# Kernel optimization log

Measured on AMD Instinct MI355X. Metric: run time of the kernel, lower is better.

Reference implementation:

```python
import jax, jax.numpy as jnp
import numpy as np

N = 50000          # nodes per node type
F = 256            # input feature dim
C = 256            # hidden_channels
H, D = 8, 32       # heads, head_dim (C = H*D)
E = 200000         # edges per edge type
OUT = 16           # out_channels
SRC = (0, 1, 0)    # edge type -> source node-type index (user,item)
DST = (1, 0, 0)    # edge type -> destination node-type index
LABELED = 1        # labeled_class = 'item'


def setup_inputs() -> dict:
    key = jax.random.key(0)
    ks = jax.random.split(key, 24)
    s = 0.06  # ~1/sqrt(256) init scale
    inp = {
        'x': jax.random.normal(ks[0], (2, N, F), jnp.float32),
        'edge_index': jax.random.randint(ks[1], (3, 2, E), 0, N, jnp.int64),
        'lin_w': jax.random.normal(ks[2], (2, F, C), jnp.float32) * s,
        'lin_b': jnp.zeros((2, C), jnp.float32),
        'k_w': jax.random.normal(ks[3], (2, C, C), jnp.float32) * s,
        'k_b': jnp.zeros((2, C), jnp.float32),
        'q_w': jax.random.normal(ks[4], (2, C, C), jnp.float32) * s,
        'q_b': jnp.zeros((2, C), jnp.float32),
        'v_w': jax.random.normal(ks[5], (2, C, C), jnp.float32) * s,
        'v_b': jnp.zeros((2, C), jnp.float32),
        'a_w': jax.random.normal(ks[6], (2, C, C), jnp.float32) * s,
        'a_b': jnp.zeros((2, C), jnp.float32),
        'skip': jnp.ones((2,), jnp.float32),
        'a_rel': jax.random.normal(ks[7], (3, H, D, D), jnp.float32) * (1.0 / np.sqrt(D)),
        'm_rel': jax.random.normal(ks[8], (3, H, D, D), jnp.float32) * (1.0 / np.sqrt(D)),
        'p_rel': jnp.ones((3, H), jnp.float32),
        'out_w': jax.random.normal(ks[9], (C, OUT), jnp.float32) * s,
        'out_b': jnp.zeros((OUT,), jnp.float32),
    }
    return inp


def _segment_softmax(alpha, idx, n):
    # alpha: [E, H], idx: [E] destination node ids
    amax = jax.ops.segment_max(alpha, idx, num_segments=n)
    amax = jnp.where(jnp.isfinite(amax), amax, 0.0)
    ex = jnp.exp(alpha - amax[idx])
    den = jax.ops.segment_sum(ex, idx, num_segments=n)
    return ex / (den[idx] + 1e-16)


def reference(x, edge_index, lin_w, lin_b, k_w, k_b, q_w, q_b, v_w, v_b,
              a_w, a_b, skip, a_rel, m_rel, p_rel, out_w, out_b):
    # per-node-type input Linear + ReLU
    h = jax.nn.relu(jnp.einsum('tnf,tfc->tnc', x, lin_w) + lin_b[:, None, :])

    def proj(w, b):
        return (jnp.einsum('tnc,tce->tne', h, w) + b[:, None, :]).reshape(2, N, H, D)

    k = proj(k_w, k_b)
    q = proj(q_w, q_b)
    v = proj(v_w, v_b)

    agg = jnp.zeros((2, N, H, D), h.dtype)
    for t in range(3):  # fixed small loop over edge types
        s, d = SRC[t], DST[t]
        src_idx, dst_idx = edge_index[t, 0], edge_index[t, 1]
        # relation-specific transforms of source keys / values
        k_rel = jnp.einsum('nhd,hde->nhe', k[s], a_rel[t])
        v_rel = jnp.einsum('nhd,hde->nhe', v[s], m_rel[t])
        # per-edge attention logits [E, H]
        alpha = (q[d][dst_idx] * k_rel[src_idx]).sum(-1) * p_rel[t] / (D ** 0.5)
        alpha = _segment_softmax(alpha, dst_idx, N)
        msg = v_rel[src_idx] * alpha[..., None]          # [E, H, D]
        agg = agg.at[d].add(jax.ops.segment_sum(msg, dst_idx, num_segments=N))

    o = agg.reshape(2, N, C)
    o = jnp.einsum('tnc,tce->tne', jax.nn.gelu(o, approximate=False), a_w) + a_b[:, None, :]
    beta = jax.nn.sigmoid(skip)[:, None, None]
    o = beta * o + (1.0 - beta) * h                      # skip connection (in == out dims)

    return o[LABELED] @ out_w + out_b                    # logits for labeled_class='item'
```

## Files before the change

kernel.cpp:

```cpp
#include <hip/hip_runtime.h>
#include <hip/hip_bf16.h>

using u16 = unsigned short;
using u32 = unsigned int;

#define NNODES 50000
#define NEDGE  200000
#define DEGCAP 64
#define NT     3125

__device__ __forceinline__ float blo2f(u32 u) { u32 v = u << 16; float f; __builtin_memcpy(&f, &v, 4); return f; }
__device__ __forceinline__ float bhi2f(u32 u) { u32 v = u & 0xffff0000u; float f; __builtin_memcpy(&f, &v, 4); return f; }
__device__ __forceinline__ u16 f2b(float f) {
  __hip_bfloat16 h = __float2bfloat16(f);
  u16 r; __builtin_memcpy(&r, &h, 2); return r;
}
__device__ __forceinline__ float gelu_exact(float x) {
  return 0.5f * x * (1.f + erff(x * 0.70710678118654752f));
}

__device__ __forceinline__ void gload16(const void* gp, void* lp) {
  __builtin_amdgcn_global_load_lds(
      (__attribute__((address_space(1))) u32*)(const_cast<void*>(gp)),
      (__attribute__((address_space(3))) u32*)lp, 16, 0, 0);
}

__device__ __forceinline__ void wait_vm0() { asm volatile("s_waitcnt vmcnt(0)" ::: "memory"); }
__device__ __forceinline__ void wait_vm2() { asm volatile("s_waitcnt vmcnt(2)" ::: "memory"); }
__device__ __forceinline__ void wait_vm4() { asm volatile("s_waitcnt vmcnt(4)" ::: "memory"); }

typedef __bf16 bh8 __attribute__((ext_vector_type(8)));
typedef float f32x4 __attribute__((ext_vector_type(4)));

struct GArg { const u16* A; const u16* B; const float* bias; u16* C; };

__device__ __forceinline__ void stage_tile(const u16* At, u16* buf, int lane) {
#pragma unroll
  for (int i = 0; i < 8; ++i) {
    const int row = i * 2 + (lane >> 5);
    const int c   = (lane & 31) ^ (row & 7);
    gload16(At + (size_t)row * 256 + c * 8, buf + i * 512 + lane * 8);
  }
}

__device__ __forceinline__ void stage_blk_bf16(const u16* At, u16* buf, int wave, int lane) {
#pragma unroll
  for (int i = 0; i < 2; ++i) {
    const int row = wave * 4 + i * 2 + (lane >> 5);
    const int c   = (lane & 31) ^ (row & 7);
    gload16(At + (size_t)row * 256 + c * 8, buf + wave * 1024 + i * 512 + lane * 8);
  }
}

__device__ __forceinline__ void stage_blk_f32(const float* At, float* buf, int wave, int lane) {
#pragma unroll
  for (int i = 0; i < 4; ++i) {
    const int row = wave * 4 + i;
    const int c   = lane ^ ((row & 7) << 1);
    gload16(At + (size_t)row * 256 + c * 4, buf + row * 256 + lane * 4);
  }
}

template <int MODE, bool F32A>
__launch_bounds__(256, 2)
__global__ void gemm_v9(GArg g0, GArg g1, GArg g2)
{
  GArg ga = (blockIdx.z == 0) ? g0 : ((blockIdx.z == 1) ? g1 : g2);
  const int tid  = threadIdx.x;
  const int lane = tid & 63;
  const int wave = tid >> 6;
  const int lr = lane & 15;
  const int lq = lane >> 4;
  const int colbase = wave * 64;

  constexpr int TW = F32A ? 8192 : 4096;
  __shared__ alignas(16) u16 lds[2][TW];
  __shared__ alignas(16) u16 pat[4][1152];
  u16* wl = &pat[wave][0];

  bh8 B[4][8];
#pragma unroll
  for (int s = 0; s < 4; ++s) {
    const u16* bp = ga.B + (size_t)(colbase + s * 16 + lr) * 256 + lq * 8;
#pragma unroll
    for (int ks = 0; ks < 8; ++ks) B[s][ks] = *(const bh8*)(bp + ks * 32);
  }
  float bias[4];
#pragma unroll
  for (int s = 0; s < 4; ++s) bias[s] = ga.bias[colbase + s * 16 + lr];

  int foff[8];
#pragma unroll
  for (int ks = 0; ks < 8; ++ks) {
    if (F32A)
      foff[ks] = lr * 256 + (((ks * 8 + lq * 2) ^ ((lr & 7) << 1)) * 4);
    else
      foff[ks] = lr * 256 + (((ks * 4 + lq) ^ (lr & 7)) * 8);
  }

  const int t0 = blockIdx.x;
  const int ts = gridDim.x;

  if (F32A) stage_blk_f32((const float*)ga.A + (size_t)t0 * 4096, (float*)&lds[0][0], wave, lane);
  else      stage_blk_bf16(ga.A + (size_t)t0 * 4096, &lds[0][0], wave, lane);
  int cur = 0;

  for (int t = t0; t < NT; t += ts) {
    const int tn = t + ts;
    if (tn < NT) {
      if (F32A) { stage_blk_f32((const float*)ga.A + (size_t)tn * 4096, (float*)&lds[cur ^ 1][0], wave, lane); wait_vm4(); }
      else      { stage_blk_bf16(ga.A + (size_t)tn * 4096, &lds[cur ^ 1][0], wave, lane); wait_vm2(); }
    } else {
      wait_vm0();
    }
    __builtin_amdgcn_s_barrier();

    bh8 ab[8];
    if (F32A) {
      const float* fbuf = (const float*)&lds[cur][0];
#pragma unroll
      for (int ks = 0; ks < 8; ++ks) {
        const f32x4 lo = *(const f32x4*)(fbuf + foff[ks]);
        const f32x4 hi = *(const f32x4*)(fbuf + foff[ks] + 4);
#pragma unroll
        for (int j = 0; j < 4; ++j) { ab[ks][j] = (__bf16)lo[j]; ab[ks][j + 4] = (__bf16)hi[j]; }
      }
    } else {
      const u16* buf = &lds[cur][0];
#pragma unroll
      for (int ks = 0; ks < 8; ++ks) ab[ks] = *(const bh8*)(buf + foff[ks]);
    }

    f32x4 acc[4];
#pragma unroll
    for (int s = 0; s < 4; ++s) acc[s] = (f32x4){0.f, 0.f, 0.f, 0.f};
#pragma unroll
    for (int ks = 0; ks < 8; ++ks) {
#pragma unroll
      for (int s = 0; s < 4; ++s)
        acc[s] = __builtin_amdgcn_mfma_f32_16x16x32_bf16(ab[ks], B[s][ks], acc[s], 0, 0, 0);
    }

#pragma unroll
    for (int s = 0; s < 4; ++s) {
#pragma unroll
      for (int r = 0; r < 4; ++r) {
        float v = acc[s][r] + bias[s];
        if (MODE == 0) v = fmaxf(v, 0.f);
        wl[(lq * 4 + r) * 72 + s * 16 + lr] = f2b(v);
      }
    }
#pragma unroll
    for (int j = 0; j < 2; ++j) {
      const int row = (lane >> 3) + j * 8;
      const int seg = lane & 7;
      const uint4 pv = *(const uint4*)(wl + row * 72 + seg * 8);
      *(uint4*)(ga.C + ((size_t)t * 16 + row) * 256 + colbase + seg * 8) = pv;
    }
    __builtin_amdgcn_s_barrier();
    cur ^= 1;
  }
}

__global__ void prep_w_k(const float* __restrict__ lin_w, const float* __restrict__ q_w,
                         const float* __restrict__ a_w, const float* __restrict__ k_w,
                         const float* __restrict__ v_w, const float* __restrict__ k_b,
                         const float* __restrict__ v_b, const float* __restrict__ a_rel,
                         const float* __restrict__ m_rel, const float* __restrict__ out_w,
                         const float* __restrict__ a_b, const float* __restrict__ out_b,
                         const float* __restrict__ skipv,
                         u16* __restrict__ lin0T, u16* __restrict__ lin1T,
                         u16* __restrict__ qT,
                         u16* __restrict__ kfT, u16* __restrict__ vfT,
                         u16* __restrict__ WcT, float* __restrict__ bfin,
                         float* __restrict__ bkf, float* __restrict__ bvf,
                         int* __restrict__ cnt)
{
  const int tid = blockIdx.x * 256 + threadIdx.x;
  const int nn = tid >> 8, kk = tid & 255;
  switch (blockIdx.y) {
    case 0: lin0T[tid] = f2b(lin_w[kk * 256 + nn]); break;
    case 1: lin1T[tid] = f2b(lin_w[65536 + kk * 256 + nn]); break;
    case 2: qT[tid] = f2b(q_w[65536 + kk * 256 + nn]); break;
    case 3: {
      const int h = nn >> 5, e = nn & 31;
      float s = 0.f;
      for (int d = 0; d < 32; ++d) s += k_w[kk * 256 + h * 32 + d] * a_rel[(h * 32 + d) * 32 + e];
      kfT[tid] = f2b(s);
      if (kk == 0) {
        float sb = 0.f;
        for (int d = 0; d < 32; ++d) sb += k_b[h * 32 + d] * a_rel[(h * 32 + d) * 32 + e];
        bkf[nn] = sb;
      }
      break;
    }
    case 4: {
      const int h = nn >> 5, e = nn & 31;
      float s = 0.f;
      for (int d = 0; d < 32; ++d) s += v_w[kk * 256 + h * 32 + d] * m_rel[(h * 32 + d) * 32 + e];
      vfT[tid] = f2b(s);
      if (kk == 0) {
        float sb = 0.f;
        for (int d = 0; d < 32; ++d) sb += v_b[h * 32 + d] * m_rel[(h * 32 + d) * 32 + e];
        bvf[nn] = sb;
      }
      break;
    }
    case 5: {
      const float beta = 1.f / (1.f + __expf(-skipv[1]));
      if (tid < 8192) {
        const int j = tid & 15;
        const int k = tid >> 4;
        float s;
        if (k < 256) {
          float acc = 0.f;
          for (int d = 0; d < 256; ++d)
            acc += a_w[65536 + k * 256 + d] * out_w[d * 16 + j];
          s = beta * acc;
        } else {
          s = (1.f - beta) * out_w[(k - 256) * 16 + j];
        }
        WcT[j * 512 + k] = f2b(s);
      }
      if (tid < 16) {
        float acc = 0.f;
        for (int c = 0; c < 256; ++c) acc += a_b[256 + c] * out_w[c * 16 + tid];
        bfin[tid] = beta * acc + out_b[tid];
      }
      break;
    }
    default:
      if (tid < NNODES) cnt[tid] = 0;
      break;
  }
}

__global__ void scatter_k(const int* __restrict__ ei, int* __restrict__ cnt, int* __restrict__ srcl) {
  const int e = blockIdx.x * 256 + threadIdx.x;
  if (e >= NEDGE) return;
  const int src = ei[e];
  const int dst = ei[NEDGE + e];
  if ((unsigned)dst >= NNODES || (unsigned)src >= NNODES) return;
  const int pos = atomicAdd(&cnt[dst], 1);
  if (pos < DEGCAP) srcl[(size_t)dst * DEGCAP + pos] = src;
}

__global__ void edge_agg_k(const u16* __restrict__ qb, const u16* __restrict__ krel,
                           const u16* __restrict__ vrel, const int* __restrict__ cnt,
                           const int* __restrict__ srcl, const float* __restrict__ prel,
                           u16* __restrict__ g)
{
  const int node = (blockIdx.x * blockDim.x + threadIdx.x) >> 6;
  if (node >= NNODES) return;
  const int lane = threadIdx.x & 63;
  const int hh = lane >> 3;
  const int off = hh * 32 + (lane & 7) * 4;
  const float scale = prel[hh] * 0.17677669529663687f;
  const uint2 qv = *(const uint2*)(qb + (size_t)node * 256 + off);
  const float q0 = blo2f(qv.x) * scale, q1 = bhi2f(qv.x) * scale;
  const float q2 = blo2f(qv.y) * scale, q3 = bhi2f(qv.y) * scale;
  int dg = cnt[node]; if (dg > DEGCAP) dg = DEGCAP;
  const int mysrc = srcl[(size_t)node * DEGCAP + lane];

  float den = 0.f, a0 = 0.f, a1 = 0.f, a2 = 0.f, a3 = 0.f;
  uint2 kv = {0, 0}, vv = {0, 0};
  if (dg > 0) {
    const int s0 = __shfl(mysrc, 0);
    kv = *(const uint2*)(krel + (size_t)s0 * 256 + off);
    vv = *(const uint2*)(vrel + (size_t)s0 * 256 + off);
  }
  for (int i = 0; i < dg; ++i) {
    uint2 kn = kv, vn = vv;
    if (i + 1 < dg) {
      const int sn = __shfl(mysrc, i + 1);
      kn = *(const uint2*)(krel + (size_t)sn * 256 + off);
      vn = *(const uint2*)(vrel + (size_t)sn * 256 + off);
    }
    float p = q0 * blo2f(kv.x) + q1 * bhi2f(kv.x) + q2 * blo2f(kv.y) + q3 * bhi2f(kv.y);
    p += __shfl_xor(p, 1);
    p += __shfl_xor(p, 2);
    p += __shfl_xor(p, 4);
    const float ex = __expf(p);
    den += ex;
    a0 += ex * blo2f(vv.x); a1 += ex * bhi2f(vv.x);
    a2 += ex * blo2f(vv.y); a3 += ex * bhi2f(vv.y);
    kv = kn; vv = vn;
  }
  float r0 = 0.f, r1 = 0.f, r2 = 0.f, r3 = 0.f;
  if (dg > 0) {
    const float inv = 1.f / den;
    r0 = gelu_exact(a0 * inv); r1 = gelu_exact(a1 * inv);
    r2 = gelu_exact(a2 * inv); r3 = gelu_exact(a3 * inv);
  }
  uint2 gv;
  gv.x = (u32)f2b(r0) | ((u32)f2b(r1) << 16);
  gv.y = (u32)f2b(r2) | ((u32)f2b(r3) << 16);
  *(uint2*)(g + (size_t)node * 256 + off) = gv;
}

__launch_bounds__(256, 2)
__global__ void final_k(const u16* __restrict__ g, const u16* __restrict__ h1,
                        const u16* __restrict__ WcT, const float* __restrict__ bfin,
                        float* __restrict__ out)
{
  const int tid = threadIdx.x;
  const int lane = tid & 63;
  const int wave = tid >> 6;
  const int lr = lane & 15;
  const int lq = lane >> 4;

  __shared__ alignas(16) u16 lds[4][8192];
  u16* buf = &lds[wave][0];

  bh8 B[16];
  {
    const u16* bp = WcT + (size_t)lr * 512 + lq * 8;
#pragma unroll
    for (int ks = 0; ks < 16; ++ks) B[ks] = *(const bh8*)(bp + ks * 32);
  }
  const float bv = bfin[lr];

  int foff[8];
#pragma unroll
  for (int ks = 0; ks < 8; ++ks)
    foff[ks] = lr * 256 + (((ks * 4 + lq) ^ (lr & 7)) * 8);

  const int wt0 = blockIdx.x * 4 + wave;
  const int wts = gridDim.x * 4;

  for (int t = wt0; t < NT; t += wts) {
    stage_tile(g  + (size_t)t * 4096, buf,        lane);
    stage_tile(h1 + (size_t)t * 4096, buf + 4096, lane);
    wait_vm0();
    f32x4 acc = {0.f, 0.f, 0.f, 0.f};
#pragma unroll
    for (int ks = 0; ks < 8; ++ks)
      acc = __builtin_amdgcn_mfma_f32_16x16x32_bf16(*(const bh8*)(buf + foff[ks]), B[ks], acc, 0, 0, 0);
#pragma unroll
    for (int ks = 0; ks < 8; ++ks)
      acc = __builtin_amdgcn_mfma_f32_16x16x32_bf16(*(const bh8*)(buf + 4096 + foff[ks]), B[ks + 8], acc, 0, 0, 0);
#pragma unroll
    for (int r = 0; r < 4; ++r)
      out[((size_t)t * 16 + lq * 4 + r) * 16 + lr] = acc[r] + bv;
  }
}

extern "C" void kernel_launch(void* const* d_in, const int* in_sizes, int n_in,
                              void* d_out, int out_size, void* d_ws, size_t ws_size,
                              hipStream_t stream)
{
  const float* x     = (const float*)d_in[0];
  const int*   ei    = (const int*)d_in[1];
  const float* lin_w = (const float*)d_in[2];
  const float* lin_b = (const float*)d_in[3];
  const float* k_w   = (const float*)d_in[4];
  const float* k_b   = (const float*)d_in[5];
  const float* q_w   = (const float*)d_in[6];
  const float* q_b   = (const float*)d_in[7];
  const float* v_w   = (const float*)d_in[8];
  const float* v_b   = (const float*)d_in[9];
  const float* a_w   = (const float*)d_in[10];
  const float* a_b   = (const float*)d_in[11];
  const float* skipv = (const float*)d_in[12];
  const float* a_rel = (const float*)d_in[13];
  const float* m_rel = (const float*)d_in[14];
  const float* p_rel = (const float*)d_in[15];
  const float* out_w = (const float*)d_in[16];
  const float* out_b = (const float*)d_in[17];
  char* ws = (char*)d_ws;

  u16*  h0    = (u16*)(ws + 0);
  u16*  h1    = (u16*)(ws + 25600000);
  u16*  qb    = (u16*)(ws + 51200000);
  u16*  krel  = (u16*)(ws + 76800000);
  u16*  vrel  = (u16*)(ws + 102400000);
  u16*  gbuf  = (u16*)(ws + 128000000);
  char* W     = ws + 153600000;
  u16*  lin0T = (u16*)(W + 0);
  u16*  lin1T = (u16*)(W + 131072);
  u16*  qT    = (u16*)(W + 2 * 131072);
  u16*  kfT   = (u16*)(W + 3 * 131072);
  u16*  vfT   = (u16*)(W + 4 * 131072);
  u16*  WcT   = (u16*)(W + 5 * 131072);
  float* bfin = (float*)(W + 5 * 131072 + 16384);
  float* bkf  = (float*)(W + 5 * 131072 + 17408);
  float* bvf  = (float*)(W + 5 * 131072 + 18432);
  int*  cnt   = (int*)(W + 5 * 131072 + 19456);
  int*  srcl  = (int*)(W + 5 * 131072 + 19456 + 200000);

  prep_w_k<<<dim3(256, 7), 256, 0, stream>>>(lin_w, q_w, a_w, k_w, v_w, k_b, v_b,
                                             a_rel, m_rel, out_w, a_b, out_b, skipv,
                                             lin0T, lin1T, qT, kfT, vfT, WcT, bfin,
                                             bkf, bvf, cnt);
  scatter_k<<<(NEDGE + 255) / 256, 256, 0, stream>>>(ei, cnt, srcl);

  {
    GArg a0{(const u16*)x, lin0T, lin_b, h0};
    GArg a1{(const u16*)(x + (size_t)NNODES * 256), lin1T, lin_b + 256, h1};
    gemm_v9<0, true><<<dim3(256, 1, 2), 256, 0, stream>>>(a0, a1, a0);
  }
  {
    GArg a0{h1, qT, q_b + 256, qb};
    GArg a1{h0, kfT, bkf, krel};
    GArg a2{h0, vfT, bvf, vrel};
    gemm_v9<1, false><<<dim3(170, 1, 3), 256, 0, stream>>>(a0, a1, a2);
  }
  edge_agg_k<<<12500, 256, 0, stream>>>(qb, krel, vrel, cnt, srcl, p_rel, gbuf);
  final_k<<<512, 256, 0, stream>>>(gbuf, h1, WcT, bfin, (float*)d_out);
}
```

Baseline: 324.2 us.

## Triple-buffer GEMM staging, split final GEMM K across waves, raise occupancy

The GEMM kernel moves from double to triple buffering, prefetching two tiles ahead with adjusted vmcnt waits. The f32 LDS swizzle changes to a 16-byte granularity with separate low and high offsets. The Q/K/V GEMM gets more blocks and a higher launch bound. The final kernel now splits K across four waves of a block, each with its own slice, reduces through LDS, and pipelines loads three-deep instead of each wave waiting synchronously. The aim is to hide global load latency and cut register pressure, at the cost of more LDS and extra barriers.

```diff
diff --git a/kernel.cpp b/kernel.cpp
--- a/kernel.cpp
+++ b/kernel.cpp
@@ -25,23 +25,12 @@
       (__attribute__((address_space(3))) u32*)lp, 16, 0, 0);
 }
 
-__device__ __forceinline__ void wait_vm0() { asm volatile("s_waitcnt vmcnt(0)" ::: "memory"); }
-__device__ __forceinline__ void wait_vm2() { asm volatile("s_waitcnt vmcnt(2)" ::: "memory"); }
-__device__ __forceinline__ void wait_vm4() { asm volatile("s_waitcnt vmcnt(4)" ::: "memory"); }
+#define WAIT_VM(N) asm volatile("s_waitcnt vmcnt(" #N ")" ::: "memory")
 
 typedef __bf16 bh8 __attribute__((ext_vector_type(8)));
 typedef float f32x4 __attribute__((ext_vector_type(4)));
 
 struct GArg { const u16* A; const u16* B; const float* bias; u16* C; };
-
-__device__ __forceinline__ void stage_tile(const u16* At, u16* buf, int lane) {
-#pragma unroll
-  for (int i = 0; i < 8; ++i) {
-    const int row = i * 2 + (lane >> 5);
-    const int c   = (lane & 31) ^ (row & 7);
-    gload16(At + (size_t)row * 256 + c * 8, buf + i * 512 + lane * 8);
-  }
-}
 
 __device__ __forceinline__ void stage_blk_bf16(const u16* At, u16* buf, int wave, int lane) {
 #pragma unroll
@@ -56,14 +45,14 @@
 #pragma unroll
   for (int i = 0; i < 4; ++i) {
     const int row = wave * 4 + i;
-    const int c   = lane ^ ((row & 7) << 1);
+    const int c   = lane ^ (row & 7);
     gload16(At + (size_t)row * 256 + c * 4, buf + row * 256 + lane * 4);
   }
 }
 
-template <int MODE, bool F32A>
-__launch_bounds__(256, 2)
-__global__ void gemm_v9(GArg g0, GArg g1, GArg g2)
+template <int MODE, bool F32A, int MAXB>
+__launch_bounds__(256, MAXB)
+__global__ void gemm_v10(GArg g0, GArg g1, GArg g2)
 {
   GArg ga = (blockIdx.z == 0) ? g0 : ((blockIdx.z == 1) ? g1 : g2);
   const int tid  = threadIdx.x;
@@ -74,7 +63,7 @@
   const int colbase = wave * 64;
 
   constexpr int TW = F32A ? 8192 : 4096;
-  __shared__ alignas(16) u16 lds[2][TW];
+  __shared__ alignas(16) u16 lds[3][TW];
   __shared__ alignas(16) u16 pat[4][1152];
   u16* wl = &pat[wave][0];
 
@@ -89,13 +78,15 @@
 #pragma unroll
   for (int s = 0; s < 4; ++s) bias[s] = ga.bias[colbase + s * 16 + lr];
 
-  int foff[8];
+  int foffL[8], foffH[8];
 #pragma unroll
   for (int ks = 0; ks < 8; ++ks) {
-    if (F32A)
-      foff[ks] = lr * 256 + (((ks * 8 + lq * 2) ^ ((lr & 7) << 1)) * 4);
-    else
-      foff[ks] = lr * 256 + (((ks * 4 + lq) ^ (lr & 7)) * 8);
+    if (F32A) {
+      foffL[ks] = lr * 256 + (((ks * 8 + lq * 2)     ^ (lr & 7)) << 2);
+      foffH[ks] = lr * 256 + (((ks * 8 + lq * 2 + 1) ^ (lr & 7)) << 2);
+    } else {
+      foffL[ks] = lr * 256 + (((ks * 4 + lq) ^ (lr & 7)) * 8);
+    }
   }
 
   const int t0 = blockIdx.x;
@@ -103,32 +94,39 @@
 
   if (F32A) stage_blk_f32((const float*)ga.A + (size_t)t0 * 4096, (float*)&lds[0][0], wave, lane);
   else      stage_blk_bf16(ga.A + (size_t)t0 * 4096, &lds[0][0], wave, lane);
-  int cur = 0;
-
-  for (int t = t0; t < NT; t += ts) {
-    const int tn = t + ts;
-    if (tn < NT) {
-      if (F32A) { stage_blk_f32((const float*)ga.A + (size_t)tn * 4096, (float*)&lds[cur ^ 1][0], wave, lane); wait_vm4(); }
-      else      { stage_blk_bf16(ga.A + (size_t)tn * 4096, &lds[cur ^ 1][0], wave, lane); wait_vm2(); }
-    } else {
-      wait_vm0();
-    }
+  if (t0 + ts < NT) {
+    if (F32A) stage_blk_f32((const float*)ga.A + (size_t)(t0 + ts) * 4096, (float*)&lds[1][0], wave, lane);
+    else      stage_blk_bf16(ga.A + (size_t)(t0 + ts) * 4096, &lds[1][0], wave, lane);
+  }
+
+  int it = 0, rb = 0;
+  for (int t = t0; t < NT; t += ts, ++it) {
+    const bool p1 = (t + ts < NT), p2 = (t + 2 * ts < NT);
+    if (p2) {
+      const int rn = (rb + 2 >= 3) ? rb - 1 : rb + 2;
+      if (F32A) stage_blk_f32((const float*)ga.A + (size_t)(t + 2 * ts) * 4096, (float*)&lds[rn][0], wave, lane);
+      else      stage_blk_bf16(ga.A + (size_t)(t + 2 * ts) * 4096, &lds[rn][0], wave, lane);
+    }
+    if (!p1)            { WAIT_VM(0); }
+    else if (!p2)       { if (F32A) { WAIT_VM(6); }  else { WAIT_VM(4); } }
+    else if (it >= 2)   { if (F32A) { WAIT_VM(12); } else { WAIT_VM(8); } }
+    else                { if (F32A) { WAIT_VM(8); }  else { WAIT_VM(4); } }
     __builtin_amdgcn_s_barrier();
 
     bh8 ab[8];
     if (F32A) {
-      const float* fbuf = (const float*)&lds[cur][0];
+      const float* fbuf = (const float*)&lds[rb][0];
 #pragma unroll
       for (int ks = 0; ks < 8; ++ks) {
-        const f32x4 lo = *(const f32x4*)(fbuf + foff[ks]);
-        const f32x4 hi = *(const f32x4*)(fbuf + foff[ks] + 4);
+        const f32x4 lo = *(const f32x4*)(fbuf + foffL[ks]);
+        const f32x4 hi = *(const f32x4*)(fbuf + foffH[ks]);
 #pragma unroll
         for (int j = 0; j < 4; ++j) { ab[ks][j] = (__bf16)lo[j]; ab[ks][j + 4] = (__bf16)hi[j]; }
       }
     } else {
-      const u16* buf = &lds[cur][0];
-#pragma unroll
-      for (int ks = 0; ks < 8; ++ks) ab[ks] = *(const bh8*)(buf + foff[ks]);
+      const u16* buf = &lds[rb][0];
+#pragma unroll
+      for (int ks = 0; ks < 8; ++ks) ab[ks] = *(const bh8*)(buf + foffL[ks]);
     }
 
     f32x4 acc[4];
@@ -158,7 +156,7 @@
       *(uint4*)(ga.C + ((size_t)t * 16 + row) * 256 + colbase + seg * 8) = pv;
     }
     __builtin_amdgcn_s_barrier();
-    cur ^= 1;
+    rb = (rb + 1 == 3) ? 0 : rb + 1;
   }
 }
 
@@ -298,10 +296,10 @@
   *(uint2*)(g + (size_t)node * 256 + off) = gv;
 }
 
-__launch_bounds__(256, 2)
-__global__ void final_k(const u16* __restrict__ g, const u16* __restrict__ h1,
-                        const u16* __restrict__ WcT, const float* __restrict__ bfin,
-                        float* __restrict__ out)
+__launch_bounds__(256, 3)
+__global__ void final_v10(const u16* __restrict__ g, const u16* __restrict__ h1,
+                          const u16* __restrict__ WcT, const float* __restrict__ bfin,
+                          float* __restrict__ out)
 {
   const int tid = threadIdx.x;
   const int lane = tid & 63;
@@ -309,40 +307,71 @@
   const int lr = lane & 15;
   const int lq = lane >> 4;
 
-  __shared__ alignas(16) u16 lds[4][8192];
-  u16* buf = &lds[wave][0];
-
-  bh8 B[16];
+  __shared__ alignas(16) u16 lds[3][8192];
+  __shared__ float red[4][256];
+
+  bh8 B[4];
   {
-    const u16* bp = WcT + (size_t)lr * 512 + lq * 8;
-#pragma unroll
-    for (int ks = 0; ks < 16; ++ks) B[ks] = *(const bh8*)(bp + ks * 32);
-  }
-  const float bv = bfin[lr];
-
-  int foff[8];
-#pragma unroll
-  for (int ks = 0; ks < 8; ++ks)
-    foff[ks] = lr * 256 + (((ks * 4 + lq) ^ (lr & 7)) * 8);
-
-  const int wt0 = blockIdx.x * 4 + wave;
-  const int wts = gridDim.x * 4;
-
-  for (int t = wt0; t < NT; t += wts) {
-    stage_tile(g  + (size_t)t * 4096, buf,        lane);
-    stage_tile(h1 + (size_t)t * 4096, buf + 4096, lane);
-    wait_vm0();
+    const u16* bp = WcT + (size_t)lr * 512 + wave * 128 + lq * 8;
+#pragma unroll
+    for (int ks = 0; ks < 4; ++ks) B[ks] = *(const bh8*)(bp + ks * 32);
+  }
+  const float bv = bfin[tid & 15];
+
+  int foff[4];
+#pragma unroll
+  for (int ks = 0; ks < 4; ++ks)
+    foff[ks] = wave * 2048 + lr * 128 + (((ks * 4 + lq) ^ (lr & 7)) * 8);
+
+  const u16* srcq = (wave < 2) ? g + wave * 128 : h1 + (wave - 2) * 128;
+
+  const int t0 = blockIdx.x;
+  const int ts = gridDim.x;
+
+#define FSTAGE(T, RB)                                                          \
+  {                                                                            \
+    _Pragma("unroll")                                                          \
+    for (int i = 0; i < 4; ++i) {                                              \
+      const int row = i * 4 + (lane >> 4);                                     \
+      const int c   = (lane & 15) ^ (row & 7);                                 \
+      gload16(srcq + (size_t)(T) * 4096 + row * 256 + c * 8,                   \
+              &lds[RB][wave * 2048 + i * 512 + lane * 8]);                     \
+    }                                                                          \
+  }
+
+  FSTAGE(t0, 0);
+  if (t0 + ts < NT) FSTAGE(t0 + ts, 1);
+
+  int it = 0, rb = 0;
+  for (int t = t0; t < NT; t += ts, ++it) {
+    const bool p1 = (t + ts < NT), p2 = (t + 2 * ts < NT);
+    if (p2) {
+      const int rn = (rb + 2 >= 3) ? rb - 1 : rb + 2;
+      FSTAGE(t + 2 * ts, rn);
+    }
+    if (!p1)          { WAIT_VM(0); }
+    else if (!p2)     { WAIT_VM(4); }
+    else if (it >= 2) { WAIT_VM(10); }
+    else              { WAIT_VM(8); }
+    __builtin_amdgcn_s_barrier();
+
     f32x4 acc = {0.f, 0.f, 0.f, 0.f};
-#pragma unroll
-    for (int ks = 0; ks < 8; ++ks)
+    const u16* buf = &lds[rb][0];
+#pragma unroll
+    for (int ks = 0; ks < 4; ++ks)
       acc = __builtin_amdgcn_mfma_f32_16x16x32_bf16(*(const bh8*)(buf + foff[ks]), B[ks], acc, 0, 0, 0);
-#pragma unroll
-    for (int ks = 0; ks < 8; ++ks)
-      acc = __builtin_amdgcn_mfma_f32_16x16x32_bf16(*(const bh8*)(buf + 4096 + foff[ks]), B[ks + 8], acc, 0, 0, 0);
-#pragma unroll
-    for (int r = 0; r < 4; ++r)
-      out[((size_t)t * 16 + lq * 4 + r) * 16 + lr] = acc[r] + bv;
-  }
+
+#pragma unroll
+    for (int r = 0; r < 4; ++r) red[wave][(lq * 4 + r) * 16 + lr] = acc[r];
+    asm volatile("s_waitcnt lgkmcnt(0)" ::: "memory");
+    __builtin_amdgcn_s_barrier();
+
+    const float s = red[0][tid] + red[1][tid] + red[2][tid] + red[3][tid] + bv;
+    out[(size_t)t * 256 + tid] = s;
+    __builtin_amdgcn_s_barrier();
+    rb = (rb + 1 == 3) ? 0 : rb + 1;
+  }
+#undef FSTAGE
 }
 
 extern "C" void kernel_launch(void* const* d_in, const int* in_sizes, int n_in,
@@ -397,14 +426,14 @@
   {
     GArg a0{(const u16*)x, lin0T, lin_b, h0};
     GArg a1{(const u16*)(x + (size_t)NNODES * 256), lin1T, lin_b + 256, h1};
-    gemm_v9<0, true><<<dim3(256, 1, 2), 256, 0, stream>>>(a0, a1, a0);
+    gemm_v10<0, true, 2><<<dim3(256, 1, 2), 256, 0, stream>>>(a0, a1, a0);
   }
   {
     GArg a0{h1, qT, q_b + 256, qb};
     GArg a1{h0, kfT, bkf, krel};
     GArg a2{h0, vfT, bvf, vrel};
-    gemm_v9<1, false><<<dim3(170, 1, 3), 256, 0, stream>>>(a0, a1, a2);
+    gemm_v10<1, false, 4><<<dim3(341, 1, 3), 256, 0, stream>>>(a0, a1, a2);
   }
   edge_agg_k<<<12500, 256, 0, stream>>>(qb, krel, vrel, cnt, srcl, p_rel, gbuf);
-  final_k<<<512, 256, 0, stream>>>(gbuf, h1, WcT, bfin, (float*)d_out);
-}
+  final_v10<<<768, 256, 0, stream>>>(gbuf, h1, WcT, bfin, (float*)d_out);
+}
```

New measurement: 384.3 us. +18.5%, slower.

## Load GEMM A-tiles directly into registers instead of staging through LDS

Applied to the files above, without the earlier changes.

The GEMM and final-projection kernels no longer stage A tiles into shared memory with global_load_lds and double-buffering. Each lane now loads its MFMA A-fragments straight from global memory into registers, which removes the LDS traffic, the swizzle offsets and the block barriers. The final kernel also raises launch bounds to 3 blocks per SM and grows its grid from 512 to 782 blocks to add occupancy. In exchange, the explicit prefetch overlap is gone, and the per-lane loads are strided 16-byte reads across rows that rely on the caches for coalescing.

```diff
diff --git a/kernel.cpp b/kernel.cpp
--- a/kernel.cpp
+++ b/kernel.cpp
@@ -19,51 +19,14 @@
   return 0.5f * x * (1.f + erff(x * 0.70710678118654752f));
 }
 
-__device__ __forceinline__ void gload16(const void* gp, void* lp) {
-  __builtin_amdgcn_global_load_lds(
-      (__attribute__((address_space(1))) u32*)(const_cast<void*>(gp)),
-      (__attribute__((address_space(3))) u32*)lp, 16, 0, 0);
-}
-
-__device__ __forceinline__ void wait_vm0() { asm volatile("s_waitcnt vmcnt(0)" ::: "memory"); }
-__device__ __forceinline__ void wait_vm2() { asm volatile("s_waitcnt vmcnt(2)" ::: "memory"); }
-__device__ __forceinline__ void wait_vm4() { asm volatile("s_waitcnt vmcnt(4)" ::: "memory"); }
-
 typedef __bf16 bh8 __attribute__((ext_vector_type(8)));
 typedef float f32x4 __attribute__((ext_vector_type(4)));
 
 struct GArg { const u16* A; const u16* B; const float* bias; u16* C; };
 
-__device__ __forceinline__ void stage_tile(const u16* At, u16* buf, int lane) {
-#pragma unroll
-  for (int i = 0; i < 8; ++i) {
-    const int row = i * 2 + (lane >> 5);
-    const int c   = (lane & 31) ^ (row & 7);
-    gload16(At + (size_t)row * 256 + c * 8, buf + i * 512 + lane * 8);
-  }
-}
-
-__device__ __forceinline__ void stage_blk_bf16(const u16* At, u16* buf, int wave, int lane) {
-#pragma unroll
-  for (int i = 0; i < 2; ++i) {
-    const int row = wave * 4 + i * 2 + (lane >> 5);
-    const int c   = (lane & 31) ^ (row & 7);
-    gload16(At + (size_t)row * 256 + c * 8, buf + wave * 1024 + i * 512 + lane * 8);
-  }
-}
-
-__device__ __forceinline__ void stage_blk_f32(const float* At, float* buf, int wave, int lane) {
-#pragma unroll
-  for (int i = 0; i < 4; ++i) {
-    const int row = wave * 4 + i;
-    const int c   = lane ^ ((row & 7) << 1);
-    gload16(At + (size_t)row * 256 + c * 4, buf + row * 256 + lane * 4);
-  }
-}
-
 template <int MODE, bool F32A>
 __launch_bounds__(256, 2)
-__global__ void gemm_v9(GArg g0, GArg g1, GArg g2)
+__global__ void gemm_v11(GArg g0, GArg g1, GArg g2)
 {
   GArg ga = (blockIdx.z == 0) ? g0 : ((blockIdx.z == 1) ? g1 : g2);
   const int tid  = threadIdx.x;
@@ -73,8 +36,6 @@
   const int lq = lane >> 4;
   const int colbase = wave * 64;
 
-  constexpr int TW = F32A ? 8192 : 4096;
-  __shared__ alignas(16) u16 lds[2][TW];
   __shared__ alignas(16) u16 pat[4][1152];
   u16* wl = &pat[wave][0];
 
@@ -89,56 +50,42 @@
 #pragma unroll
   for (int s = 0; s < 4; ++s) bias[s] = ga.bias[colbase + s * 16 + lr];
 
-  int foff[8];
-#pragma unroll
-  for (int ks = 0; ks < 8; ++ks) {
-    if (F32A)
-      foff[ks] = lr * 256 + (((ks * 8 + lq * 2) ^ ((lr & 7) << 1)) * 4);
-    else
-      foff[ks] = lr * 256 + (((ks * 4 + lq) ^ (lr & 7)) * 8);
-  }
-
   const int t0 = blockIdx.x;
   const int ts = gridDim.x;
 
-  if (F32A) stage_blk_f32((const float*)ga.A + (size_t)t0 * 4096, (float*)&lds[0][0], wave, lane);
-  else      stage_blk_bf16(ga.A + (size_t)t0 * 4096, &lds[0][0], wave, lane);
-  int cur = 0;
-
   for (int t = t0; t < NT; t += ts) {
-    const int tn = t + ts;
-    if (tn < NT) {
-      if (F32A) { stage_blk_f32((const float*)ga.A + (size_t)tn * 4096, (float*)&lds[cur ^ 1][0], wave, lane); wait_vm4(); }
-      else      { stage_blk_bf16(ga.A + (size_t)tn * 4096, &lds[cur ^ 1][0], wave, lane); wait_vm2(); }
+    f32x4 acc[4];
+#pragma unroll
+    for (int s = 0; s < 4; ++s) acc[s] = (f32x4){0.f, 0.f, 0.f, 0.f};
+
+    if (F32A) {
+      const float* ap = (const float*)ga.A + ((size_t)t * 16 + lr) * 256 + lq * 8;
+      f32x4 lo[8], hi[8];
+#pragma unroll
+      for (int ks = 0; ks < 8; ++ks) {
+        lo[ks] = *(const f32x4*)(ap + ks * 32);
+        hi[ks] = *(const f32x4*)(ap + ks * 32 + 4);
+      }
+#pragma unroll
+      for (int ks = 0; ks < 8; ++ks) {
+        bh8 a;
+#pragma unroll
+        for (int j = 0; j < 4; ++j) { a[j] = (__bf16)lo[ks][j]; a[j + 4] = (__bf16)hi[ks][j]; }
+#pragma unroll
+        for (int s = 0; s < 4; ++s)
+          acc[s] = __builtin_amdgcn_mfma_f32_16x16x32_bf16(a, B[s][ks], acc[s], 0, 0, 0);
+      }
     } else {
-      wait_vm0();
-    }
-    __builtin_amdgcn_s_barrier();
-
-    bh8 ab[8];
-    if (F32A) {
-      const float* fbuf = (const float*)&lds[cur][0];
+      const u16* ap = ga.A + ((size_t)t * 16 + lr) * 256 + lq * 8;
+      bh8 ab[8];
+#pragma unroll
+      for (int ks = 0; ks < 8; ++ks) ab[ks] = *(const bh8*)(ap + ks * 32);
 #pragma unroll
       for (int ks = 0; ks < 8; ++ks) {
-        const f32x4 lo = *(const f32x4*)(fbuf + foff[ks]);
-        const f32x4 hi = *(const f32x4*)(fbuf + foff[ks] + 4);
-#pragma unroll
-        for (int j = 0; j < 4; ++j) { ab[ks][j] = (__bf16)lo[j]; ab[ks][j + 4] = (__bf16)hi[j]; }
-      }
-    } else {
-      const u16* buf = &lds[cur][0];
-#pragma unroll
-      for (int ks = 0; ks < 8; ++ks) ab[ks] = *(const bh8*)(buf + foff[ks]);
-    }
-
-    f32x4 acc[4];
-#pragma unroll
-    for (int s = 0; s < 4; ++s) acc[s] = (f32x4){0.f, 0.f, 0.f, 0.f};
-#pragma unroll
-    for (int ks = 0; ks < 8; ++ks) {
-#pragma unroll
-      for (int s = 0; s < 4; ++s)
-        acc[s] = __builtin_amdgcn_mfma_f32_16x16x32_bf16(ab[ks], B[s][ks], acc[s], 0, 0, 0);
+#pragma unroll
+        for (int s = 0; s < 4; ++s)
+          acc[s] = __builtin_amdgcn_mfma_f32_16x16x32_bf16(ab[ks], B[s][ks], acc[s], 0, 0, 0);
+      }
     }
 
 #pragma unroll
@@ -157,8 +104,6 @@
       const uint4 pv = *(const uint4*)(wl + row * 72 + seg * 8);
       *(uint4*)(ga.C + ((size_t)t * 16 + row) * 256 + colbase + seg * 8) = pv;
     }
-    __builtin_amdgcn_s_barrier();
-    cur ^= 1;
   }
 }
 
@@ -298,10 +243,10 @@
   *(uint2*)(g + (size_t)node * 256 + off) = gv;
 }
 
-__launch_bounds__(256, 2)
-__global__ void final_k(const u16* __restrict__ g, const u16* __restrict__ h1,
-                        const u16* __restrict__ WcT, const float* __restrict__ bfin,
-                        float* __restrict__ out)
+__launch_bounds__(256, 3)
+__global__ void final_v11(const u16* __restrict__ g, const u16* __restrict__ h1,
+                          const u16* __restrict__ WcT, const float* __restrict__ bfin,
+                          float* __restrict__ out)
 {
   const int tid = threadIdx.x;
   const int lane = tid & 63;
@@ -309,9 +254,6 @@
   const int lr = lane & 15;
   const int lq = lane >> 4;
 
-  __shared__ alignas(16) u16 lds[4][8192];
-  u16* buf = &lds[wave][0];
-
   bh8 B[16];
   {
     const u16* bp = WcT + (size_t)lr * 512 + lq * 8;
@@ -320,25 +262,23 @@
   }
   const float bv = bfin[lr];
 
-  int foff[8];
-#pragma unroll
-  for (int ks = 0; ks < 8; ++ks)
-    foff[ks] = lr * 256 + (((ks * 4 + lq) ^ (lr & 7)) * 8);
-
   const int wt0 = blockIdx.x * 4 + wave;
   const int wts = gridDim.x * 4;
 
   for (int t = wt0; t < NT; t += wts) {
-    stage_tile(g  + (size_t)t * 4096, buf,        lane);
-    stage_tile(h1 + (size_t)t * 4096, buf + 4096, lane);
-    wait_vm0();
+    const u16* gp = g  + ((size_t)t * 16 + lr) * 256 + lq * 8;
+    const u16* hp = h1 + ((size_t)t * 16 + lr) * 256 + lq * 8;
+    bh8 a[16];
+#pragma unroll
+    for (int ks = 0; ks < 8; ++ks) a[ks]     = *(const bh8*)(gp + ks * 32);
+#pragma unroll
+    for (int ks = 0; ks < 8; ++ks) a[8 + ks] = *(const bh8*)(hp + ks * 32);
+
     f32x4 acc = {0.f, 0.f, 0.f, 0.f};
 #pragma unroll
-    for (int ks = 0; ks < 8; ++ks)
-      acc = __builtin_amdgcn_mfma_f32_16x16x32_bf16(*(const bh8*)(buf + foff[ks]), B[ks], acc, 0, 0, 0);
-#pragma unroll
-    for (int ks = 0; ks < 8; ++ks)
-      acc = __builtin_amdgcn_mfma_f32_16x16x32_bf16(*(const bh8*)(buf + 4096 + foff[ks]), B[ks + 8], acc, 0, 0, 0);
+    for (int ks = 0; ks < 16; ++ks)
+      acc = __builtin_amdgcn_mfma_f32_16x16x32_bf16(a[ks], B[ks], acc, 0, 0, 0);
+
 #pragma unroll
     for (int r = 0; r < 4; ++r)
       out[((size_t)t * 16 + lq * 4 + r) * 16 + lr] = acc[r] + bv;
@@ -397,14 +337,14 @@
   {
     GArg a0{(const u16*)x, lin0T, lin_b, h0};
     GArg a1{(const u16*)(x + (size_t)NNODES * 256), lin1T, lin_b + 256, h1};
-    gemm_v9<0, true><<<dim3(256, 1, 2), 256, 0, stream>>>(a0, a1, a0);
+    gemm_v11<0, true><<<dim3(256, 1, 2), 256, 0, stream>>>(a0, a1, a0);
   }
   {
     GArg a0{h1, qT, q_b + 256, qb};
     GArg a1{h0, kfT, bkf, krel};
     GArg a2{h0, vfT, bvf, vrel};
-    gemm_v9<1, false><<<dim3(170, 1, 3), 256, 0, stream>>>(a0, a1, a2);
+    gemm_v11<1, false><<<dim3(170, 1, 3), 256, 0, stream>>>(a0, a1, a2);
   }
   edge_agg_k<<<12500, 256, 0, stream>>>(qb, krel, vrel, cnt, srcl, p_rel, gbuf);
-  final_k<<<512, 256, 0, stream>>>(gbuf, h1, WcT, bfin, (float*)d_out);
-}
+  final_v11<<<782, 256, 0, stream>>>(gbuf, h1, WcT, bfin, (float*)d_out);
+}
```

New measurement: 383.6 us. 1.18x slower.
